# Optimization experiments

Measured on AMD Instinct MI355X. Metric: run time of the kernel, lower is better.

## Reference

```python
import jax, jax.numpy as jnp
import numpy as np

WS = 8          # window size
NH = 8          # num heads
DIM = 256
HD = DIM // NH  # head dim = 32
SCALE = HD ** -0.5
EPS = 1e-5


def _rel_pos_index(ws):
    # deterministic int index buffer, same math as the torch __init__
    coords = jnp.stack(jnp.meshgrid(jnp.arange(ws), jnp.arange(ws), indexing='ij'))  # [2,ws,ws]
    cf = coords.reshape(2, -1)                     # [2, N]
    rel = cf[:, :, None] - cf[:, None, :]          # [2, N, N]
    return (rel[0] + ws - 1) * (2 * ws - 1) + (rel[1] + ws - 1)  # [N, N]


def _ln(h, g, b):
    m = jnp.mean(h, axis=-1, keepdims=True)
    v = jnp.mean((h - m) ** 2, axis=-1, keepdims=True)
    return (h - m) / jnp.sqrt(v + EPS) * g + b


def setup_inputs() -> dict:
    key = jax.random.key(0)
    ks = jax.random.split(key, 16)
    B_, N, D = 4096, WS * WS, DIM
    s = 0.02
    return {
        'x':      jax.random.normal(ks[0], (B_, N, D), jnp.float32),
        # enhanced qkv: Linear(D,2D) -> LN -> GELU -> Linear(2D,3D)
        'w_qkv1': jax.random.normal(ks[1], (D, 2 * D), jnp.float32) * s,
        'b_qkv1': jnp.zeros((2 * D,), jnp.float32),
        'g_qkv':  jnp.ones((2 * D,), jnp.float32),
        'be_qkv': jnp.zeros((2 * D,), jnp.float32),
        'w_qkv2': jax.random.normal(ks[2], (2 * D, 3 * D), jnp.float32) * s,
        'b_qkv2': jnp.zeros((3 * D,), jnp.float32),
        # relative position bias table [(2*WS-1)^2, NH]
        'rpb':    jax.random.normal(ks[3], ((2 * WS - 1) ** 2, NH), jnp.float32) * s,
        # enhanced proj: Linear(D,2D) -> LN -> GELU -> Linear(2D,D)
        'w_p1':   jax.random.normal(ks[4], (D, 2 * D), jnp.float32) * s,
        'b_p1':   jnp.zeros((2 * D,), jnp.float32),
        'g_p':    jnp.ones((2 * D,), jnp.float32),
        'be_p':   jnp.zeros((2 * D,), jnp.float32),
        'w_p2':   jax.random.normal(ks[5], (2 * D, D), jnp.float32) * s,
        'b_p2':   jnp.zeros((D,), jnp.float32),
    }


def reference(x, w_qkv1, b_qkv1, g_qkv, be_qkv, w_qkv2, b_qkv2, rpb,
              w_p1, b_p1, g_p, be_p, w_p2, b_p2):
    B_, N, C = x.shape
    # enhanced QKV chain: Linear -> LayerNorm -> GELU -> Linear
    h = jax.nn.gelu(_ln(x @ w_qkv1 + b_qkv1, g_qkv, be_qkv), approximate=False)
    qkv = h @ w_qkv2 + b_qkv2                              # [B_, N, 3C]
    qkv = qkv.reshape(B_, N, 3, NH, HD).transpose(2, 0, 3, 1, 4)  # [3, B_, H, N, hd]
    q, k, v = qkv[0], qkv[1], qkv[2]
    attn = jnp.einsum('bhnd,bhmd->bhnm', q * SCALE, k)     # [B_, H, N, N]
    idx = _rel_pos_index(WS)                                # [N, N] int
    bias = rpb[idx.reshape(-1)].reshape(N, N, NH).transpose(2, 0, 1)  # [H, N, N]
    attn = jax.nn.softmax(attn + bias[None], axis=-1)
    out = jnp.einsum('bhnm,bhmd->bhnd', attn, v)           # [B_, H, N, hd]
    out = out.transpose(0, 2, 1, 3).reshape(B_, N, C)
    # enhanced proj chain: Linear -> LayerNorm -> GELU -> Linear
    h = jax.nn.gelu(_ln(out @ w_p1 + b_p1, g_p, be_p), approximate=False)
    return h @ w_p2 + b_p2
```

## Files before the change

kernel.cpp:

```cpp
#include <hip/hip_runtime.h>


typedef __bf16 bf16_t;
typedef __bf16 bf16x8 __attribute__((ext_vector_type(8)));
typedef __bf16 bf16x4 __attribute__((ext_vector_type(4)));
typedef float f32x4 __attribute__((ext_vector_type(4)));

__device__ __forceinline__ f32x4 mfma16(bf16x8 a, bf16x8 b, f32x4 acc) {
  return __builtin_amdgcn_mfma_f32_16x16x32_bf16(a, b, acc, 0, 0, 0);
}

#define SWZ(row, byteoff) ((byteoff) ^ (((row) & 7) << 4))

__device__ __forceinline__ float gelu_f(float v) {
  float e = __expf(v * (1.59576912f + 0.07135482f * v * v));
  return v - v * __builtin_amdgcn_rcpf(1.0f + e);
}

__global__ void prep_kernel(const float* __restrict__ w1, const float* __restrict__ w2,
                            const float* __restrict__ wp1, const float* __restrict__ wp2,
                            const float* __restrict__ rpb,
                            bf16_t* __restrict__ w1t, bf16_t* __restrict__ w2t,
                            bf16_t* __restrict__ wp1t, bf16_t* __restrict__ wp2t,
                            float* __restrict__ bt) {
  int i = blockIdx.x * 256 + threadIdx.x;
  if (i < 131072) {
    int k = i & 255, n = i >> 8;
    w1t[i] = (bf16_t)w1[k * 512 + n];
    return;
  }
  i -= 131072;
  if (i < 393216) {
    int k = i & 511, n = i >> 9;
    w2t[i] = (bf16_t)w2[k * 768 + n];
    return;
  }
  i -= 393216;
  if (i < 131072) {
    int k = i & 255, n = i >> 8;
    wp1t[i] = (bf16_t)wp1[k * 512 + n];
    return;
  }
  i -= 131072;
  if (i < 131072) {
    int k = i & 511, n = i >> 9;
    wp2t[i] = (bf16_t)wp2[k * 256 + n];
    return;
  }
  i -= 131072;
  if (i < 32768) {
    int hd = i >> 12, r = (i >> 6) & 63, j = i & 63;
    int idx = ((r >> 3) - (j >> 3) + 7) * 15 + ((r & 7) - (j & 7) + 7);
    bt[i] = rpb[idx * 8 + hd];
  }
}

__device__ __forceinline__ void gemmT_ln_gelu16(
    const char* bsrc, const bf16_t* __restrict__ wt,
    const float* __restrict__ bias, const float* __restrict__ gamma,
    const float* __restrict__ beta,
    char* dst, int flb, float2* part, int wave, int g, int c)
{
  f32x4 acc[2][4] = {};
#pragma unroll
  for (int kt = 0; kt < 8; ++kt) {
    bf16x8 a[2], b[4];
#pragma unroll
    for (int mt = 0; mt < 2; ++mt)
      a[mt] = *(const bf16x8*)(wt + (size_t)(wave * 32 + mt * 16 + c) * 256 + kt * 32 + g * 8);
#pragma unroll
    for (int nt = 0; nt < 4; ++nt) {
      int T = nt * 16 + c;
      b[nt] = *(const bf16x8*)(bsrc + SWZ(T, T * 512 + kt * 64 + g * 16));
    }
#pragma unroll
    for (int mt = 0; mt < 2; ++mt)
#pragma unroll
      for (int nt = 0; nt < 4; ++nt)
        acc[mt][nt] = mfma16(a[mt], b[nt], acc[mt][nt]);
  }
  float s[4] = {0.f, 0.f, 0.f, 0.f}, ss[4] = {0.f, 0.f, 0.f, 0.f};
#pragma unroll
  for (int mt = 0; mt < 2; ++mt) {
    float4 b4 = *(const float4*)(bias + wave * 32 + mt * 16 + g * 4);
#pragma unroll
    for (int nt = 0; nt < 4; ++nt)
#pragma unroll
      for (int r = 0; r < 4; ++r) {
        float v = acc[mt][nt][r] + ((const float*)&b4)[r];
        acc[mt][nt][r] = v;
        s[nt] += v;
        ss[nt] += v * v;
      }
  }
#pragma unroll
  for (int nt = 0; nt < 4; ++nt) {
    float sv = s[nt], ssv = ss[nt];
    sv += __shfl_xor(sv, 16, 64); ssv += __shfl_xor(ssv, 16, 64);
    sv += __shfl_xor(sv, 32, 64); ssv += __shfl_xor(ssv, 32, 64);
    if (g == 0) part[wave * 64 + nt * 16 + c] = make_float2(sv, ssv);
  }
  __syncthreads();
#pragma unroll
  for (int nt = 0; nt < 4; ++nt) {
    float sv = 0.f, ssv = 0.f;
#pragma unroll
    for (int w = 0; w < 16; ++w) {
      float2 p2 = part[w * 64 + nt * 16 + c];
      sv += p2.x; ssv += p2.y;
    }
    float m = sv * (1.f / 512.f);
    float rstd = rsqrtf(ssv * (1.f / 512.f) - m * m + 1e-5f);
#pragma unroll
    for (int mt = 0; mt < 2; ++mt)
#pragma unroll
      for (int r = 0; r < 4; ++r)
        acc[mt][nt][r] = (acc[mt][nt][r] - m) * rstd;
  }
#pragma unroll
  for (int mt = 0; mt < 2; ++mt) {
    float4 g4 = *(const float4*)(gamma + wave * 32 + mt * 16 + g * 4);
    float4 be4 = *(const float4*)(beta + wave * 32 + mt * 16 + g * 4);
    int f0 = flb + mt * 16 + g * 4;
#pragma unroll
    for (int nt = 0; nt < 4; ++nt) {
      int T = nt * 16 + c;
      bf16x4 h4;
#pragma unroll
      for (int r = 0; r < 4; ++r) {
        float v = acc[mt][nt][r] * ((const float*)&g4)[r] + ((const float*)&be4)[r];
        h4[r] = (bf16_t)gelu_f(v);
      }
      *(bf16x4*)(dst + SWZ(T, T * 512 + f0 * 2)) = h4;
    }
  }
}

__global__ __launch_bounds__(1024, 1) void g1qa_kernel(
    const float* __restrict__ x,
    const bf16_t* __restrict__ w1t, const float* __restrict__ b1,
    const float* __restrict__ gamma1, const float* __restrict__ beta1,
    const bf16_t* __restrict__ w2t, const float* __restrict__ b2,
    const float* __restrict__ bt,
    bf16_t* __restrict__ ao)
{
  __shared__ __align__(16) char sm[163840];
  char* rA = sm;
  char* rB = sm + 32768;
  float2* part = (float2*)(sm + 65536);
  const int tid = threadIdx.x;
  const int wave = tid >> 6, lane = tid & 63;
  const int g = lane >> 4, c = lane & 15;
  const int win = blockIdx.x;

  const float* xw = x + (size_t)win * 16384;
#pragma unroll
  for (int it = 0; it < 4; ++it) {
    int e = it * 4096 + tid * 4;
    float4 v = *(const float4*)(xw + e);
    int row = e >> 8, col = e & 255;
    bf16x4 t4;
    t4[0] = (bf16_t)v.x; t4[1] = (bf16_t)v.y; t4[2] = (bf16_t)v.z; t4[3] = (bf16_t)v.w;
    *(bf16x4*)(rA + SWZ(row, row * 512 + col * 2)) = t4;
  }
  __syncthreads();
  gemmT_ln_gelu16(rA, w1t, b1, gamma1, beta1, (wave < 8) ? rB : rA, (wave & 7) * 32,
                  part, wave, g, c);
  __syncthreads();

  const int hh = wave >> 1, mh = wave & 1;
  {
    f32x4 accv[4] = {}, accq[4] = {}, acck[4] = {};
    const bf16_t* wq = w2t + (size_t)(hh * 32 + mh * 16 + c) * 512;
    const bf16_t* wk = wq + (size_t)256 * 512;
    const bf16_t* wv = wq + (size_t)512 * 512;
#pragma unroll
    for (int kt = 0; kt < 16; ++kt) {
      const char* hb = (kt < 8) ? rB : rA;
      const int ko = (kt & 7) * 64 + g * 16;
      bf16x8 av = *(const bf16x8*)(wv + kt * 32 + g * 8);
      bf16x8 aq = *(const bf16x8*)(wq + kt * 32 + g * 8);
      bf16x8 ak = *(const bf16x8*)(wk + kt * 32 + g * 8);
      bf16x8 b[4];
#pragma unroll
      for (int nt = 0; nt < 4; ++nt) {
        int T = nt * 16 + c;
        b[nt] = *(const bf16x8*)(hb + SWZ(T, T * 512 + ko));
      }
#pragma unroll
      for (int nt = 0; nt < 4; ++nt) {
        accv[nt] = mfma16(av, b[nt], accv[nt]);
        accq[nt] = mfma16(aq, b[nt], accq[nt]);
        acck[nt] = mfma16(ak, b[nt], acck[nt]);
      }
    }
    float4 bv4 = *(const float4*)(b2 + 512 + hh * 32 + mh * 16 + g * 4);
    float4 bq4 = *(const float4*)(b2 + hh * 32 + mh * 16 + g * 4);
    float4 bk4 = *(const float4*)(b2 + 256 + hh * 32 + mh * 16 + g * 4);
    char* qb = sm + 65536 + hh * 8192;
    char* vs = sm + 131072 + hh * 4096;
    const int d0 = mh * 16 + g * 4;
#pragma unroll
    for (int nt = 0; nt < 4; ++nt) {
      int T = nt * 16 + c;
      bf16x4 q4, k4;
#pragma unroll
      for (int r = 0; r < 4; ++r) {
        q4[r] = (bf16_t)((accq[nt][r] + ((const float*)&bq4)[r]) * 0.17677669529663687f);
        k4[r] = (bf16_t)(acck[nt][r] + ((const float*)&bk4)[r]);
      }
      *(bf16x4*)(qb + SWZ(T, T * 64 + d0 * 2)) = q4;
      *(bf16x4*)(qb + 4096 + SWZ(T, T * 64 + d0 * 2)) = k4;
#pragma unroll
      for (int r = 0; r < 4; ++r) {
        int d = d0 + r;
        *(bf16_t*)(vs + SWZ(d, d * 128 + T * 2)) =
            (bf16_t)(accv[nt][r] + ((const float*)&bv4)[r]);
      }
    }
  }
  __syncthreads();

  const int h8 = wave & 7, rowbase = (wave >> 3) * 32;
  char* qb = sm + 65536 + h8 * 8192;
  char* vslot = sm + 131072 + h8 * 4096;
  const float* btab = bt + h8 * 4096;

  bf16x8 aq[2], bk[4];
#pragma unroll
  for (int mt = 0; mt < 2; ++mt) {
    int t = rowbase + mt * 16 + c;
    aq[mt] = *(const bf16x8*)(qb + SWZ(t, t * 64 + g * 16));
  }
#pragma unroll
  for (int nt = 0; nt < 4; ++nt) {
    int t = nt * 16 + c;
    bk[nt] = *(const bf16x8*)(qb + 4096 + SWZ(t, t * 64 + g * 16));
  }
  float p[2][4][4];
#pragma unroll
  for (int mt = 0; mt < 2; ++mt)
#pragma unroll
    for (int nt = 0; nt < 4; ++nt) {
      f32x4 z = {0.f, 0.f, 0.f, 0.f};
      f32x4 s4 = mfma16(aq[mt], bk[nt], z);
#pragma unroll
      for (int r = 0; r < 4; ++r) {
        int i = rowbase + mt * 16 + g * 4 + r, j = nt * 16 + c;
        p[mt][nt][r] = s4[r] + btab[i * 64 + j];
      }
    }
#pragma unroll
  for (int mt = 0; mt < 2; ++mt)
#pragma unroll
    for (int r = 0; r < 4; ++r) {
      float mx = fmaxf(fmaxf(p[mt][0][r], p[mt][1][r]), fmaxf(p[mt][2][r], p[mt][3][r]));
#pragma unroll
      for (int m = 1; m < 16; m <<= 1) mx = fmaxf(mx, __shfl_xor(mx, m, 64));
      float sum = 0.f;
#pragma unroll
      for (int nt = 0; nt < 4; ++nt) {
        float e = __expf(p[mt][nt][r] - mx);
        p[mt][nt][r] = e; sum += e;
      }
#pragma unroll
      for (int m = 1; m < 16; m <<= 1) sum += __shfl_xor(sum, m, 64);
      float rinv = 1.f / sum;
#pragma unroll
      for (int nt = 0; nt < 4; ++nt) p[mt][nt][r] *= rinv;
    }
  __syncthreads();

#pragma unroll
  for (int mt = 0; mt < 2; ++mt)
#pragma unroll
    for (int nt = 0; nt < 4; ++nt)
#pragma unroll
      for (int r = 0; r < 4; ++r) {
        int i = rowbase + mt * 16 + g * 4 + r, j = nt * 16 + c;
        *(bf16_t*)(qb + SWZ(i, i * 128 + j * 2)) = (bf16_t)p[mt][nt][r];
      }
  asm volatile("s_waitcnt lgkmcnt(0)" ::: "memory");
  f32x4 oacc[2][2] = {};
#pragma unroll
  for (int kp = 0; kp < 2; ++kp) {
    bf16x8 ap[2], bv[2];
#pragma unroll
    for (int mt = 0; mt < 2; ++mt) {
      int t = rowbase + mt * 16 + c;
      ap[mt] = *(const bf16x8*)(qb + SWZ(t, t * 128 + kp * 64 + g * 16));
    }
#pragma unroll
    for (int nt = 0; nt < 2; ++nt) {
      int d = nt * 16 + c;
      bv[nt] = *(const bf16x8*)(vslot + SWZ(d, d * 128 + kp * 64 + g * 16));
    }
#pragma unroll
    for (int mt = 0; mt < 2; ++mt)
#pragma unroll
      for (int nt = 0; nt < 2; ++nt)
        oacc[mt][nt] = mfma16(ap[mt], bv[nt], oacc[mt][nt]);
  }
#pragma unroll
  for (int mt = 0; mt < 2; ++mt)
#pragma unroll
    for (int nt = 0; nt < 2; ++nt)
#pragma unroll
      for (int r = 0; r < 4; ++r) {
        int T = rowbase + mt * 16 + g * 4 + r;
        ao[(size_t)(win * 64 + T) * 256 + h8 * 32 + nt * 16 + c] = (bf16_t)oacc[mt][nt][r];
      }
}

__global__ __launch_bounds__(1024, 1) void g3g4_kernel(
    const bf16_t* __restrict__ ao,
    const bf16_t* __restrict__ wp1t, const float* __restrict__ bp1,
    const float* __restrict__ gp, const float* __restrict__ bep,
    const bf16_t* __restrict__ wp2t, const float* __restrict__ bp2,
    float* __restrict__ out)
{
  __shared__ __align__(16) char sm[73728];
  char* rA = sm;
  char* rB = sm + 32768;
  float2* part = (float2*)(sm + 65536);
  const int tid = threadIdx.x;
  const int wave = tid >> 6, lane = tid & 63;
  const int g = lane >> 4, c = lane & 15;
  const int win = blockIdx.x;

  const bf16_t* aow = ao + (size_t)win * 16384;
#pragma unroll
  for (int it = 0; it < 2; ++it) {
    int e = it * 8192 + tid * 8;
    bf16x8 v = *(const bf16x8*)(aow + e);
    int row = e >> 8, col = e & 255;
    *(bf16x8*)(rA + SWZ(row, row * 512 + col * 2)) = v;
  }
  __syncthreads();
  gemmT_ln_gelu16(rA, wp1t, bp1, gp, bep, (wave < 8) ? rB : rA, (wave & 7) * 32,
                  part, wave, g, c);
  __syncthreads();

  f32x4 acc[4] = {};
#pragma unroll
  for (int kt = 0; kt < 16; ++kt) {
    const char* hb = (kt < 8) ? rB : rA;
    const int ko = (kt & 7) * 64 + g * 16;
    bf16x8 a = *(const bf16x8*)(wp2t + (size_t)(wave * 16 + c) * 512 + kt * 32 + g * 8);
    bf16x8 b[4];
#pragma unroll
    for (int nt = 0; nt < 4; ++nt) {
      int T = nt * 16 + c;
      b[nt] = *(const bf16x8*)(hb + SWZ(T, T * 512 + ko));
    }
#pragma unroll
    for (int nt = 0; nt < 4; ++nt)
      acc[nt] = mfma16(a, b[nt], acc[nt]);
  }
  float* ow = out + (size_t)win * 16384;
  float4 b4 = *(const float4*)(bp2 + wave * 16 + g * 4);
#pragma unroll
  for (int nt = 0; nt < 4; ++nt) {
    int T = nt * 16 + c;
    f32x4 o4;
#pragma unroll
    for (int r = 0; r < 4; ++r) o4[r] = acc[nt][r] + ((const float*)&b4)[r];
    *(f32x4*)(ow + T * 256 + wave * 16 + g * 4) = o4;
  }
}

extern "C" void kernel_launch(void* const* d_in, const int* in_sizes, int n_in,
                              void* d_out, int out_size, void* d_ws, size_t ws_size,
                              hipStream_t stream) {
  const float* x   = (const float*)d_in[0];
  const float* w1  = (const float*)d_in[1];
  const float* b1  = (const float*)d_in[2];
  const float* g1  = (const float*)d_in[3];
  const float* be1 = (const float*)d_in[4];
  const float* w2  = (const float*)d_in[5];
  const float* b2  = (const float*)d_in[6];
  const float* rpb = (const float*)d_in[7];
  const float* wp1 = (const float*)d_in[8];
  const float* bp1 = (const float*)d_in[9];
  const float* gp  = (const float*)d_in[10];
  const float* bep = (const float*)d_in[11];
  const float* wp2 = (const float*)d_in[12];
  const float* bp2 = (const float*)d_in[13];
  float* out = (float*)d_out;
  char* ws = (char*)d_ws;
  bf16_t* w1t  = (bf16_t*)(ws + 0);
  bf16_t* w2t  = (bf16_t*)(ws + 262144);
  bf16_t* wp1t = (bf16_t*)(ws + 1048576);
  bf16_t* wp2t = (bf16_t*)(ws + 1310720);
  float*  bt   = (float*)(ws + 1572864);
  bf16_t* ao   = (bf16_t*)(ws + 2097152);

  prep_kernel<<<3200, 256, 0, stream>>>(w1, w2, wp1, wp2, rpb,
                                        w1t, w2t, wp1t, wp2t, bt);

  g1qa_kernel<<<4096, 1024, 0, stream>>>(x, w1t, b1, g1, be1, w2t, b2, bt, ao);
  g3g4_kernel<<<4096, 1024, 0, stream>>>(ao, wp1t, bp1, gp, bep, wp2t, bp2, out);
}
```

Baseline: 1.077 ms.

## Fuse attention and projection kernels into one per-window mega kernel

Merges the QKV+attention kernel and the projection-MLP kernel into a single kernel, keeping the per-window attention output in shared memory instead of writing it to a global bf16 buffer and reading it back. LDS regions are reassigned so the attention output, the second hidden buffers and the LayerNorm partials do not overlap live data. This removes one launch and a global round-trip of the intermediate. The cost is a longer kernel with the larger LDS footprint held throughout, which may affect scheduling or register pressure.

```diff
diff --git a/kernel.cpp b/kernel.cpp
--- a/kernel.cpp
+++ b/kernel.cpp
@@ -136,18 +136,25 @@
   }
 }
 
-__global__ __launch_bounds__(1024, 1) void g1qa_kernel(
+__global__ __launch_bounds__(1024, 1) void mega_kernel(
     const float* __restrict__ x,
     const bf16_t* __restrict__ w1t, const float* __restrict__ b1,
     const float* __restrict__ gamma1, const float* __restrict__ beta1,
     const bf16_t* __restrict__ w2t, const float* __restrict__ b2,
     const float* __restrict__ bt,
-    bf16_t* __restrict__ ao)
+    const bf16_t* __restrict__ wp1t, const float* __restrict__ bp1,
+    const float* __restrict__ gp, const float* __restrict__ bep,
+    const bf16_t* __restrict__ wp2t, const float* __restrict__ bp2,
+    float* __restrict__ out)
 {
   __shared__ __align__(16) char sm[163840];
   char* rA = sm;
   char* rB = sm + 32768;
-  float2* part = (float2*)(sm + 65536);
+  float2* part1 = (float2*)(sm + 65536);
+  char* aoS = sm;
+  char* rB2 = sm + 65536;
+  char* rA2 = sm + 98304;
+  float2* part2 = (float2*)(sm + 131072);
   const int tid = threadIdx.x;
   const int wave = tid >> 6, lane = tid & 63;
   const int g = lane >> 4, c = lane & 15;
@@ -165,7 +172,7 @@
   }
   __syncthreads();
   gemmT_ln_gelu16(rA, w1t, b1, gamma1, beta1, (wave < 8) ? rB : rA, (wave & 7) * 32,
-                  part, wave, g, c);
+                  part1, wave, g, c);
   __syncthreads();
 
   const int hh = wave >> 1, mh = wave & 1;
@@ -221,151 +228,135 @@
   }
   __syncthreads();
 
-  const int h8 = wave & 7, rowbase = (wave >> 3) * 32;
-  char* qb = sm + 65536 + h8 * 8192;
-  char* vslot = sm + 131072 + h8 * 4096;
-  const float* btab = bt + h8 * 4096;
-
-  bf16x8 aq[2], bk[4];
-#pragma unroll
-  for (int mt = 0; mt < 2; ++mt) {
-    int t = rowbase + mt * 16 + c;
-    aq[mt] = *(const bf16x8*)(qb + SWZ(t, t * 64 + g * 16));
-  }
-#pragma unroll
-  for (int nt = 0; nt < 4; ++nt) {
-    int t = nt * 16 + c;
-    bk[nt] = *(const bf16x8*)(qb + 4096 + SWZ(t, t * 64 + g * 16));
-  }
-  float p[2][4][4];
-#pragma unroll
-  for (int mt = 0; mt < 2; ++mt)
-#pragma unroll
-    for (int nt = 0; nt < 4; ++nt) {
-      f32x4 z = {0.f, 0.f, 0.f, 0.f};
-      f32x4 s4 = mfma16(aq[mt], bk[nt], z);
-#pragma unroll
-      for (int r = 0; r < 4; ++r) {
-        int i = rowbase + mt * 16 + g * 4 + r, j = nt * 16 + c;
-        p[mt][nt][r] = s4[r] + btab[i * 64 + j];
-      }
-    }
-#pragma unroll
-  for (int mt = 0; mt < 2; ++mt)
-#pragma unroll
-    for (int r = 0; r < 4; ++r) {
-      float mx = fmaxf(fmaxf(p[mt][0][r], p[mt][1][r]), fmaxf(p[mt][2][r], p[mt][3][r]));
-#pragma unroll
-      for (int m = 1; m < 16; m <<= 1) mx = fmaxf(mx, __shfl_xor(mx, m, 64));
-      float sum = 0.f;
-#pragma unroll
-      for (int nt = 0; nt < 4; ++nt) {
-        float e = __expf(p[mt][nt][r] - mx);
-        p[mt][nt][r] = e; sum += e;
-      }
-#pragma unroll
-      for (int m = 1; m < 16; m <<= 1) sum += __shfl_xor(sum, m, 64);
-      float rinv = 1.f / sum;
-#pragma unroll
-      for (int nt = 0; nt < 4; ++nt) p[mt][nt][r] *= rinv;
-    }
-  __syncthreads();
-
-#pragma unroll
-  for (int mt = 0; mt < 2; ++mt)
-#pragma unroll
-    for (int nt = 0; nt < 4; ++nt)
-#pragma unroll
-      for (int r = 0; r < 4; ++r) {
-        int i = rowbase + mt * 16 + g * 4 + r, j = nt * 16 + c;
-        *(bf16_t*)(qb + SWZ(i, i * 128 + j * 2)) = (bf16_t)p[mt][nt][r];
-      }
-  asm volatile("s_waitcnt lgkmcnt(0)" ::: "memory");
-  f32x4 oacc[2][2] = {};
-#pragma unroll
-  for (int kp = 0; kp < 2; ++kp) {
-    bf16x8 ap[2], bv[2];
+  {
+    const int h8 = wave & 7, rowbase = (wave >> 3) * 32;
+    char* qb = sm + 65536 + h8 * 8192;
+    char* vslot = sm + 131072 + h8 * 4096;
+    const float* btab = bt + h8 * 4096;
+
+    bf16x8 aq[2], bk[4];
 #pragma unroll
     for (int mt = 0; mt < 2; ++mt) {
       int t = rowbase + mt * 16 + c;
-      ap[mt] = *(const bf16x8*)(qb + SWZ(t, t * 128 + kp * 64 + g * 16));
-    }
-#pragma unroll
-    for (int nt = 0; nt < 2; ++nt) {
-      int d = nt * 16 + c;
-      bv[nt] = *(const bf16x8*)(vslot + SWZ(d, d * 128 + kp * 64 + g * 16));
+      aq[mt] = *(const bf16x8*)(qb + SWZ(t, t * 64 + g * 16));
+    }
+#pragma unroll
+    for (int nt = 0; nt < 4; ++nt) {
+      int t = nt * 16 + c;
+      bk[nt] = *(const bf16x8*)(qb + 4096 + SWZ(t, t * 64 + g * 16));
+    }
+    float p[2][4][4];
+#pragma unroll
+    for (int mt = 0; mt < 2; ++mt)
+#pragma unroll
+      for (int nt = 0; nt < 4; ++nt) {
+        f32x4 z = {0.f, 0.f, 0.f, 0.f};
+        f32x4 s4 = mfma16(aq[mt], bk[nt], z);
+#pragma unroll
+        for (int r = 0; r < 4; ++r) {
+          int i = rowbase + mt * 16 + g * 4 + r, j = nt * 16 + c;
+          p[mt][nt][r] = s4[r] + btab[i * 64 + j];
+        }
+      }
+#pragma unroll
+    for (int mt = 0; mt < 2; ++mt)
+#pragma unroll
+      for (int r = 0; r < 4; ++r) {
+        float mx = fmaxf(fmaxf(p[mt][0][r], p[mt][1][r]), fmaxf(p[mt][2][r], p[mt][3][r]));
+#pragma unroll
+        for (int m = 1; m < 16; m <<= 1) mx = fmaxf(mx, __shfl_xor(mx, m, 64));
+        float sum = 0.f;
+#pragma unroll
+        for (int nt = 0; nt < 4; ++nt) {
+          float e = __expf(p[mt][nt][r] - mx);
+          p[mt][nt][r] = e; sum += e;
+        }
+#pragma unroll
+        for (int m = 1; m < 16; m <<= 1) sum += __shfl_xor(sum, m, 64);
+        float rinv = 1.f / sum;
+#pragma unroll
+        for (int nt = 0; nt < 4; ++nt) p[mt][nt][r] *= rinv;
+      }
+    __syncthreads();
+
+#pragma unroll
+    for (int mt = 0; mt < 2; ++mt)
+#pragma unroll
+      for (int nt = 0; nt < 4; ++nt)
+#pragma unroll
+        for (int r = 0; r < 4; ++r) {
+          int i = rowbase + mt * 16 + g * 4 + r, j = nt * 16 + c;
+          *(bf16_t*)(qb + SWZ(i, i * 128 + j * 2)) = (bf16_t)p[mt][nt][r];
+        }
+    asm volatile("s_waitcnt lgkmcnt(0)" ::: "memory");
+    f32x4 oacc[2][2] = {};
+#pragma unroll
+    for (int kp = 0; kp < 2; ++kp) {
+      bf16x8 ap[2], bv[2];
+#pragma unroll
+      for (int mt = 0; mt < 2; ++mt) {
+        int t = rowbase + mt * 16 + c;
+        ap[mt] = *(const bf16x8*)(qb + SWZ(t, t * 128 + kp * 64 + g * 16));
+      }
+#pragma unroll
+      for (int nt = 0; nt < 2; ++nt) {
+        int d = nt * 16 + c;
+        bv[nt] = *(const bf16x8*)(vslot + SWZ(d, d * 128 + kp * 64 + g * 16));
+      }
+#pragma unroll
+      for (int mt = 0; mt < 2; ++mt)
+#pragma unroll
+        for (int nt = 0; nt < 2; ++nt)
+          oacc[mt][nt] = mfma16(ap[mt], bv[nt], oacc[mt][nt]);
     }
 #pragma unroll
     for (int mt = 0; mt < 2; ++mt)
 #pragma unroll
       for (int nt = 0; nt < 2; ++nt)
-        oacc[mt][nt] = mfma16(ap[mt], bv[nt], oacc[mt][nt]);
-  }
-#pragma unroll
-  for (int mt = 0; mt < 2; ++mt)
-#pragma unroll
-    for (int nt = 0; nt < 2; ++nt)
-#pragma unroll
-      for (int r = 0; r < 4; ++r) {
-        int T = rowbase + mt * 16 + g * 4 + r;
-        ao[(size_t)(win * 64 + T) * 256 + h8 * 32 + nt * 16 + c] = (bf16_t)oacc[mt][nt][r];
-      }
-}
-
-__global__ __launch_bounds__(1024, 1) void g3g4_kernel(
-    const bf16_t* __restrict__ ao,
-    const bf16_t* __restrict__ wp1t, const float* __restrict__ bp1,
-    const float* __restrict__ gp, const float* __restrict__ bep,
-    const bf16_t* __restrict__ wp2t, const float* __restrict__ bp2,
-    float* __restrict__ out)
-{
-  __shared__ __align__(16) char sm[73728];
-  char* rA = sm;
-  char* rB = sm + 32768;
-  float2* part = (float2*)(sm + 65536);
-  const int tid = threadIdx.x;
-  const int wave = tid >> 6, lane = tid & 63;
-  const int g = lane >> 4, c = lane & 15;
-  const int win = blockIdx.x;
-
-  const bf16_t* aow = ao + (size_t)win * 16384;
-#pragma unroll
-  for (int it = 0; it < 2; ++it) {
-    int e = it * 8192 + tid * 8;
-    bf16x8 v = *(const bf16x8*)(aow + e);
-    int row = e >> 8, col = e & 255;
-    *(bf16x8*)(rA + SWZ(row, row * 512 + col * 2)) = v;
-  }
-  __syncthreads();
-  gemmT_ln_gelu16(rA, wp1t, bp1, gp, bep, (wave < 8) ? rB : rA, (wave & 7) * 32,
-                  part, wave, g, c);
-  __syncthreads();
-
-  f32x4 acc[4] = {};
-#pragma unroll
-  for (int kt = 0; kt < 16; ++kt) {
-    const char* hb = (kt < 8) ? rB : rA;
-    const int ko = (kt & 7) * 64 + g * 16;
-    bf16x8 a = *(const bf16x8*)(wp2t + (size_t)(wave * 16 + c) * 512 + kt * 32 + g * 8);
-    bf16x8 b[4];
+#pragma unroll
+        for (int r = 0; r < 4; ++r) {
+          int T = rowbase + mt * 16 + g * 4 + r;
+          int f = h8 * 32 + nt * 16 + c;
+          *(bf16_t*)(aoS + SWZ(T, T * 512 + f * 2)) = (bf16_t)oacc[mt][nt][r];
+        }
+  }
+  __syncthreads();
+
+  __builtin_amdgcn_sched_barrier(0);
+
+  gemmT_ln_gelu16(aoS, wp1t, bp1, gp, bep, (wave < 8) ? rB2 : rA2, (wave & 7) * 32,
+                  part2, wave, g, c);
+  __syncthreads();
+
+  __builtin_amdgcn_sched_barrier(0);
+
+  {
+    f32x4 acc[4] = {};
+#pragma unroll
+    for (int kt = 0; kt < 16; ++kt) {
+      const char* hb = (kt < 8) ? rB2 : rA2;
+      const int ko = (kt & 7) * 64 + g * 16;
+      bf16x8 a = *(const bf16x8*)(wp2t + (size_t)(wave * 16 + c) * 512 + kt * 32 + g * 8);
+      bf16x8 b[4];
+#pragma unroll
+      for (int nt = 0; nt < 4; ++nt) {
+        int T = nt * 16 + c;
+        b[nt] = *(const bf16x8*)(hb + SWZ(T, T * 512 + ko));
+      }
+#pragma unroll
+      for (int nt = 0; nt < 4; ++nt)
+        acc[nt] = mfma16(a, b[nt], acc[nt]);
+    }
+    float* ow = out + (size_t)win * 16384;
+    float4 b4 = *(const float4*)(bp2 + wave * 16 + g * 4);
 #pragma unroll
     for (int nt = 0; nt < 4; ++nt) {
       int T = nt * 16 + c;
-      b[nt] = *(const bf16x8*)(hb + SWZ(T, T * 512 + ko));
-    }
-#pragma unroll
-    for (int nt = 0; nt < 4; ++nt)
-      acc[nt] = mfma16(a, b[nt], acc[nt]);
-  }
-  float* ow = out + (size_t)win * 16384;
-  float4 b4 = *(const float4*)(bp2 + wave * 16 + g * 4);
-#pragma unroll
-  for (int nt = 0; nt < 4; ++nt) {
-    int T = nt * 16 + c;
-    f32x4 o4;
-#pragma unroll
-    for (int r = 0; r < 4; ++r) o4[r] = acc[nt][r] + ((const float*)&b4)[r];
-    *(f32x4*)(ow + T * 256 + wave * 16 + g * 4) = o4;
+      f32x4 o4;
+#pragma unroll
+      for (int r = 0; r < 4; ++r) o4[r] = acc[nt][r] + ((const float*)&b4)[r];
+      *(f32x4*)(ow + T * 256 + wave * 16 + g * 4) = o4;
+    }
   }
 }
 
@@ -393,11 +384,10 @@
   bf16_t* wp1t = (bf16_t*)(ws + 1048576);
   bf16_t* wp2t = (bf16_t*)(ws + 1310720);
   float*  bt   = (float*)(ws + 1572864);
-  bf16_t* ao   = (bf16_t*)(ws + 2097152);
 
   prep_kernel<<<3200, 256, 0, stream>>>(w1, w2, wp1, wp2, rpb,
                                         w1t, w2t, wp1t, wp2t, bt);
 
-  g1qa_kernel<<<4096, 1024, 0, stream>>>(x, w1t, b1, g1, be1, w2t, b2, bt, ao);
-  g3g4_kernel<<<4096, 1024, 0, stream>>>(ao, wp1t, bp1, gp, bep, wp2t, bp2, out);
-}
+  mega_kernel<<<4096, 1024, 0, stream>>>(x, w1t, b1, g1, be1, w2t, b2, bt,
+                                         wp1t, bp1, gp, bep, wp2t, bp2, out);
+}
```

Result: slower. 1.141 ms (+5.9%).
